# Kernel tuning notes

Hardware: AMD Instinct MI355X
Metric: run time of the kernel (lower is better)

Reference implementation:

```python
import jax, jax.numpy as jnp
import numpy as np

DIM = 320
HEADS = 8
GROUPS = 32
KV_DIM = 768


def group_norm(x, scale, bias, groups=GROUPS, eps=1e-6):
    b, c, h, w = x.shape
    xg = x.reshape(b, groups, c // groups, h, w)
    mu = xg.mean(axis=(2, 3, 4), keepdims=True)
    var = xg.var(axis=(2, 3, 4), keepdims=True)
    xg = (xg - mu) * jax.lax.rsqrt(var + eps)
    x = xg.reshape(b, c, h, w)
    return x * scale[None, :, None, None] + bias[None, :, None, None]


def layer_norm(x, scale, bias, eps=1e-5):
    mu = x.mean(-1, keepdims=True)
    var = x.var(-1, keepdims=True)
    return (x - mu) * jax.lax.rsqrt(var + eps) * scale + bias


def cross_attention(x, kv, wq, wk, wv, wo, bo, heads=HEADS):
    # weights stored as [in, out] (transposed vs torch Linear)
    b, lq, d = x.shape
    lk = kv.shape[1]
    dh = d // heads
    q = (x @ wq).reshape(b, lq, heads, dh).transpose(0, 2, 1, 3)
    k = (kv @ wk).reshape(b, lk, heads, dh).transpose(0, 2, 1, 3)
    v = (kv @ wv).reshape(b, lk, heads, dh).transpose(0, 2, 1, 3)
    scores = jnp.einsum('bhqd,bhkd->bhqk', q, k) * (dh ** -0.5)
    attn = jax.nn.softmax(scores, axis=-1)
    out = jnp.einsum('bhqk,bhkd->bhqd', attn, v)
    out = out.transpose(0, 2, 1, 3).reshape(b, lq, d)
    return out @ wo + bo


def setup_inputs() -> dict:
    key = jax.random.key(0)
    ks = jax.random.split(key, 24)
    d = DIM
    s = 0.02
    inp = {
        'q': jax.random.normal(ks[0], (2, d, 64, 64), jnp.float32),
        'kv': jax.random.normal(ks[1], (2, 77, KV_DIM), jnp.float32),
        'gn_s': jnp.ones((d,), jnp.float32),
        'gn_b': jnp.zeros((d,), jnp.float32),
        'cin_w': jax.random.normal(ks[2], (d, d), jnp.float32) * s,
        'cin_b': jnp.zeros((d,), jnp.float32),
        'ln0_s': jnp.ones((d,), jnp.float32),
        'ln0_b': jnp.zeros((d,), jnp.float32),
        'a1_wq': jax.random.normal(ks[3], (d, d), jnp.float32) * s,
        'a1_wk': jax.random.normal(ks[4], (d, d), jnp.float32) * s,
        'a1_wv': jax.random.normal(ks[5], (d, d), jnp.float32) * s,
        'a1_wo': jax.random.normal(ks[6], (d, d), jnp.float32) * s,
        'a1_bo': jnp.zeros((d,), jnp.float32),
        'ln1_s': jnp.ones((d,), jnp.float32),
        'ln1_b': jnp.zeros((d,), jnp.float32),
        'a2_wq': jax.random.normal(ks[7], (d, d), jnp.float32) * s,
        'a2_wk': jax.random.normal(ks[8], (KV_DIM, d), jnp.float32) * s,
        'a2_wv': jax.random.normal(ks[9], (KV_DIM, d), jnp.float32) * s,
        'a2_wo': jax.random.normal(ks[10], (d, d), jnp.float32) * s,
        'a2_bo': jnp.zeros((d,), jnp.float32),
        'lnA_s': jnp.ones((d,), jnp.float32),
        'lnA_b': jnp.zeros((d,), jnp.float32),
        'fc0_w': jax.random.normal(ks[11], (d, 8 * d), jnp.float32) * s,
        'fc0_b': jnp.zeros((8 * d,), jnp.float32),
        'fc1_w': jax.random.normal(ks[12], (4 * d, d), jnp.float32) * s,
        'fc1_b': jnp.zeros((d,), jnp.float32),
        'cout_w': jax.random.normal(ks[13], (d, d), jnp.float32) * s,
        'cout_b': jnp.zeros((d,), jnp.float32),
    }
    return inp


def reference(q, kv, gn_s, gn_b, cin_w, cin_b, ln0_s, ln0_b,
              a1_wq, a1_wk, a1_wv, a1_wo, a1_bo, ln1_s, ln1_b,
              a2_wq, a2_wk, a2_wv, a2_wo, a2_bo, lnA_s, lnA_b,
              fc0_w, fc0_b, fc1_w, fc1_b, cout_w, cout_b):
    b, c, h, w = q.shape
    res1 = q
    x = group_norm(q, gn_s, gn_b)
    # 1x1 conv == channel matmul
    x = jnp.einsum('bchw,co->bohw', x, cin_w) + cin_b[None, :, None, None]
    x = x.transpose(0, 2, 3, 1).reshape(b, h * w, c)
    xn = layer_norm(x, ln0_s, ln0_b)
    x = cross_attention(xn, xn, a1_wq, a1_wk, a1_wv, a1_wo, a1_bo) + x
    x = cross_attention(layer_norm(x, ln1_s, ln1_b), kv,
                        a2_wq, a2_wk, a2_wv, a2_wo, a2_bo) + x
    res2 = x
    g = layer_norm(x, lnA_s, lnA_b) @ fc0_w + fc0_b
    half = g.shape[-1] // 2
    # GEGLU: value * GELU(gate); torch nn.GELU default is exact (erf)
    g = g[..., :half] * jax.nn.gelu(g[..., half:], approximate=False)
    x = g @ fc1_w + fc1_b + res2
    x = x.reshape(b, h, w, c).transpose(0, 3, 1, 2)
    x = jnp.einsum('bchw,co->bohw', x, cout_w) + cout_b[None, :, None, None] + res1
    return x
```

## Files before the change

kernel.cpp:

```cpp
#include <hip/hip_runtime.h>
#include <math.h>

typedef short short8 __attribute__((ext_vector_type(8)));
typedef float floatx4 __attribute__((ext_vector_type(4)));
typedef unsigned short ushort_t;
typedef unsigned int uint_t;

constexpr int BATCH   = 2;
constexpr int DIM     = 320;
constexpr int NHEADS  = 8;
constexpr int DH      = 40;
constexpr int NGROUPS = 32;
constexpr int CPG     = 10;
constexpr int SPATIAL = 4096;
constexpr int ROWS    = BATCH * SPATIAL;
constexpr int KVL     = 77;
constexpr int KVD     = 768;
constexpr int FF      = 1280;
constexpr int TQ      = 128;
constexpr int SELF_PARTS = 4;

#define QK_EXP2_SCALE 0.2281259062f

__device__ __forceinline__ ushort_t f2bf(float f) {
    uint_t u = __float_as_uint(f);
    u += 0x7FFFu + ((u >> 16) & 1u);
    return (ushort_t)(u >> 16);
}
__device__ __forceinline__ float bf2f(ushort_t u) {
    return __uint_as_float(((uint_t)u) << 16);
}

__device__ __forceinline__ void gld16(const ushort_t* g, ushort_t* l) {
    __builtin_amdgcn_global_load_lds(
        (const __attribute__((address_space(1))) void*)g,
        (__attribute__((address_space(3))) void*)l, 16, 0, 0);
}

__global__ __launch_bounds__(256) void gn_partial_kernel(const float* __restrict__ q,
                                                         float* __restrict__ stats) {
    int slice = blockIdx.x, bg = blockIdx.y;
    const float* base = q + (size_t)bg * (CPG * SPATIAL) + slice * 2560;
    float s = 0.f, ss = 0.f;
#pragma unroll
    for (int j = 0; j < 10; j++) {
        float v = base[j * 256 + threadIdx.x];
        s += v; ss += v * v;
    }
    __shared__ float rs[256], rss[256];
    rs[threadIdx.x] = s; rss[threadIdx.x] = ss;
    __syncthreads();
    for (int off = 128; off > 0; off >>= 1) {
        if (threadIdx.x < off) {
            rs[threadIdx.x]  += rs[threadIdx.x + off];
            rss[threadIdx.x] += rss[threadIdx.x + off];
        }
        __syncthreads();
    }
    if (threadIdx.x == 0) {
        atomicAdd(&stats[bg * 2],     rs[0]);
        atomicAdd(&stats[bg * 2 + 1], rss[0]);
    }
}

__global__ void gn_apply_transpose_kernel(const float* __restrict__ q,
                                          const float* __restrict__ stats,
                                          const float* __restrict__ gs,
                                          const float* __restrict__ gb,
                                          ushort_t* __restrict__ out) {
    __shared__ float tile[32][33];
    int l0 = blockIdx.x * 32, c0 = blockIdx.y * 32, b = blockIdx.z;
    int tx = threadIdx.x, ty = threadIdx.y;
    int c = c0 + ty;
    int g = c / CPG;
    float s  = stats[(b * NGROUPS + g) * 2];
    float ss = stats[(b * NGROUPS + g) * 2 + 1];
    const float invn = 1.f / 40960.f;
    float mean = s * invn;
    float rstd = rsqrtf(ss * invn - mean * mean + 1e-6f);
    float v = q[((size_t)(b * DIM + c)) * SPATIAL + l0 + tx];
    tile[ty][tx] = (v - mean) * rstd * gs[c] + gb[c];
    __syncthreads();
    out[((size_t)(b * SPATIAL + l0 + ty)) * DIM + c0 + tx] = f2bf(tile[tx][ty]);
}

__global__ __launch_bounds__(256) void ln_kernel(const float* __restrict__ x,
                                                 const float* __restrict__ sc,
                                                 const float* __restrict__ bi,
                                                 ushort_t* __restrict__ out) {
    int row = blockIdx.x * 4 + (threadIdx.x >> 6);
    int lane = threadIdx.x & 63;
    const float* xr = x + (size_t)row * DIM;
    float v[5];
    float sum = 0.f, sq = 0.f;
#pragma unroll
    for (int j = 0; j < 5; j++) {
        v[j] = xr[lane + j * 64];
        sum += v[j]; sq += v[j] * v[j];
    }
#pragma unroll
    for (int off = 32; off > 0; off >>= 1) {
        sum += __shfl_down(sum, off);
        sq  += __shfl_down(sq, off);
    }
    sum = __shfl(sum, 0); sq = __shfl(sq, 0);
    float mean = sum / (float)DIM;
    float rstd = rsqrtf(sq / (float)DIM - mean * mean + 1e-5f);
#pragma unroll
    for (int j = 0; j < 5; j++) {
        int i = lane + j * 64;
        out[(size_t)row * DIM + i] = f2bf((v[j] - mean) * rstd * sc[i] + bi[i]);
    }
}

struct WSeg { const float* src; ushort_t* dst; int K; int N; int t0; };
struct WTab {
    WSeg s[12];
    const float* cvt_src; ushort_t* cvt_dst; int cvt_n; int cvt_t0;
    float* stats;
};

__global__ __launch_bounds__(256) void wtrans_all_kernel(WTab tab) {
    int bid = blockIdx.x;
    if (bid >= tab.cvt_t0) {
        int local = bid - tab.cvt_t0;
        int base = local * 8192;
#pragma unroll
        for (int j = 0; j < 32; j++) {
            int i = base + j * 256 + threadIdx.x;
            if (i < tab.cvt_n) tab.cvt_dst[i] = f2bf(tab.cvt_src[i]);
        }
        if (local == 0 && threadIdx.x < 128) tab.stats[threadIdx.x] = 0.f;
        return;
    }
    __shared__ float tile[32][33];
    int si = 0;
#pragma unroll
    for (int i = 1; i < 12; i++) if (bid >= tab.s[i].t0) si = i;
    WSeg sg = tab.s[si];
    int local = bid - sg.t0;
    int ntn = sg.N >> 5;
    int kt = local / ntn, nt = local - kt * ntn;
    int n0 = nt * 32, k0 = kt * 32;
    int tx = threadIdx.x & 31, ty8 = threadIdx.x >> 5;
    for (int r = ty8; r < 32; r += 8)
        tile[r][tx] = sg.src[(size_t)(k0 + r) * sg.N + n0 + tx];
    __syncthreads();
    for (int r = ty8; r < 32; r += 8)
        sg.dst[(size_t)(n0 + r) * sg.K + k0 + tx] = f2bf(tile[tx][r]);
}

__global__ __launch_bounds__(256) void vtrans_kernel(const ushort_t* __restrict__ src,
                                                     ushort_t* __restrict__ dst,
                                                     int stride, int headOff,
                                                     int L, int Lpad) {
    __shared__ ushort_t tile[32][41];
    int bh = blockIdx.y, b = bh >> 3, h = bh & 7;
    int l0 = blockIdx.x * 32;
    for (int idx = threadIdx.x; idx < 32 * 40; idx += 256) {
        int l = idx / 40, d = idx - l * 40;
        ushort_t v = 0;
        if (l0 + l < L)
            v = src[(size_t)(b * L + l0 + l) * stride + headOff + h * DH + d];
        tile[l][d] = v;
    }
    __syncthreads();
    for (int idx = threadIdx.x; idx < 48 * 32; idx += 256) {
        int d = idx >> 5, li = idx & 31;
        ushort_t v;
        if (d < 40)      v = tile[li][d];
        else if (d == 40) v = 0x3F80;
        else             v = 0;
        dst[((size_t)bh * 48 + d) * Lpad + l0 + li] = v;
    }
}

template <int TM>
__global__ __launch_bounds__(256) void gemm_bf16_kernel(
    const ushort_t* __restrict__ A, const ushort_t* __restrict__ Wt,
    const float* __restrict__ bias, const float* __restrict__ resid,
    float* __restrict__ Cf, ushort_t* __restrict__ Cb,
    int M, int N, int K, float qsc, int ncut)
{
    constexpr int G = TM / 64;
    __shared__ __align__(16) ushort_t As[TM][64];
    __shared__ __align__(16) ushort_t Bs[64][64];
    int tid = threadIdx.x;
    int wave = tid >> 6, lane = tid & 63;
    int l15 = tid & 15, quad = lane >> 4;
    int m0 = blockIdx.x * TM, n0 = blockIdx.y * 64;
    int lrow = lane >> 3, slot = lane & 7;
    floatx4 acc[G][4] = {};

    for (int k0 = 0; k0 < K; k0 += 64) {
#pragma unroll
        for (int t = 0; t < TM / 32; t++) {
            int task = wave * (TM / 32) + t;
            int r = task * 8 + lrow;
            int gc = slot ^ (r & 7);
            gld16(&A[(size_t)(m0 + r) * K + k0 + gc * 8], &As[task * 8][0]);
        }
#pragma unroll
        for (int t = 0; t < 2; t++) {
            int task = wave * 2 + t;
            int r = task * 8 + lrow;
            int gc = slot ^ (r & 7);
            gld16(&Wt[(size_t)(n0 + r) * K + k0 + gc * 8], &Bs[task * 8][0]);
        }
        __syncthreads();
        short8 a[G][2], b[4][2];
#pragma unroll
        for (int g = 0; g < G; g++) {
            int r = (TM / 4) * wave + 16 * g + l15;
            a[g][0] = *(const short8*)&As[r][(quad ^ (r & 7)) * 8];
            a[g][1] = *(const short8*)&As[r][((4 + quad) ^ (r & 7)) * 8];
        }
#pragma unroll
        for (int t = 0; t < 4; t++) {
            int r = 16 * t + l15;
            b[t][0] = *(const short8*)&Bs[r][(quad ^ (r & 7)) * 8];
            b[t][1] = *(const short8*)&Bs[r][((4 + quad) ^ (r & 7)) * 8];
        }
#pragma unroll
        for (int g = 0; g < G; g++)
#pragma unroll
            for (int t = 0; t < 4; t++) {
                acc[g][t] = __builtin_amdgcn_mfma_f32_16x16x32_bf16(a[g][0], b[t][0], acc[g][t], 0, 0, 0);
                acc[g][t] = __builtin_amdgcn_mfma_f32_16x16x32_bf16(a[g][1], b[t][1], acc[g][t], 0, 0, 0);
            }
        __syncthreads();
    }

#pragma unroll
    for (int g = 0; g < G; g++) {
        int mrow = m0 + (TM / 4) * wave + 16 * g + quad * 4;
#pragma unroll
        for (int t = 0; t < 4; t++) {
            int n = n0 + 16 * t + l15;
            float bv = bias ? bias[n] : 0.f;
            float sc = (n < ncut) ? qsc : 1.f;
#pragma unroll
            for (int i = 0; i < 4; i++) {
                int m = mrow + i;
                float v = acc[g][t][i] + bv;
                if (resid) v += resid[(size_t)m * N + n];
                v *= sc;
                if (Cf) Cf[(size_t)m * N + n] = v;
                if (Cb) Cb[(size_t)m * N + n] = f2bf(v);
            }
        }
    }
}

__global__ __launch_bounds__(256) void geglu128_kernel(
    const ushort_t* __restrict__ A, const ushort_t* __restrict__ Wt,
    const float* __restrict__ bias, ushort_t* __restrict__ C, int M)
{
    constexpr int K = 320;
    __shared__ __align__(16) ushort_t As[128][64];
    __shared__ __align__(16) ushort_t Bv[64][64];
    __shared__ __align__(16) ushort_t Bg[64][64];
    int tid = threadIdx.x;
    int wave = tid >> 6, lane = tid & 63;
    int l15 = tid & 15, quad = lane >> 4;
    int m0 = blockIdx.x * 128, n0 = blockIdx.y * 64;
    int lrow = lane >> 3, slot = lane & 7;
    floatx4 av[2][4] = {}, ag[2][4] = {};

    for (int k0 = 0; k0 < K; k0 += 64) {
#pragma unroll
        for (int t = 0; t < 4; t++) {
            int task = wave * 4 + t;
            int r = task * 8 + lrow;
            int gc = slot ^ (r & 7);
            gld16(&A[(size_t)(m0 + r) * K + k0 + gc * 8], &As[task * 8][0]);
        }
#pragma unroll
        for (int t = 0; t < 2; t++) {
            int task = wave * 2 + t;
            int r = task * 8 + lrow;
            int gc = slot ^ (r & 7);
            gld16(&Wt[(size_t)(n0 + r) * K + k0 + gc * 8],      &Bv[task * 8][0]);
            gld16(&Wt[(size_t)(FF + n0 + r) * K + k0 + gc * 8], &Bg[task * 8][0]);
        }
        __syncthreads();
        short8 a[2][2], bv[4][2], bg[4][2];
#pragma unroll
        for (int g = 0; g < 2; g++) {
            int r = 32 * wave + 16 * g + l15;
            a[g][0] = *(const short8*)&As[r][(quad ^ (r & 7)) * 8];
            a[g][1] = *(const short8*)&As[r][((4 + quad) ^ (r & 7)) * 8];
        }
#pragma unroll
        for (int t = 0; t < 4; t++) {
            int r = 16 * t + l15;
            bv[t][0] = *(const short8*)&Bv[r][(quad ^ (r & 7)) * 8];
            bv[t][1] = *(const short8*)&Bv[r][((4 + quad) ^ (r & 7)) * 8];
            bg[t][0] = *(const short8*)&Bg[r][(quad ^ (r & 7)) * 8];
            bg[t][1] = *(const short8*)&Bg[r][((4 + quad) ^ (r & 7)) * 8];
        }
#pragma unroll
        for (int g = 0; g < 2; g++)
#pragma unroll
            for (int t = 0; t < 4; t++) {
                av[g][t] = __builtin_amdgcn_mfma_f32_16x16x32_bf16(a[g][0], bv[t][0], av[g][t], 0, 0, 0);
                av[g][t] = __builtin_amdgcn_mfma_f32_16x16x32_bf16(a[g][1], bv[t][1], av[g][t], 0, 0, 0);
                ag[g][t] = __builtin_amdgcn_mfma_f32_16x16x32_bf16(a[g][0], bg[t][0], ag[g][t], 0, 0, 0);
                ag[g][t] = __builtin_amdgcn_mfma_f32_16x16x32_bf16(a[g][1], bg[t][1], ag[g][t], 0, 0, 0);
            }
        __syncthreads();
    }

#pragma unroll
    for (int g = 0; g < 2; g++) {
        int mrow = m0 + 32 * wave + 16 * g + quad * 4;
#pragma unroll
        for (int t = 0; t < 4; t++) {
            int n = n0 + 16 * t + l15;
            float bb = bias[n], bgte = bias[FF + n];
#pragma unroll
            for (int i = 0; i < 4; i++) {
                float val  = av[g][t][i] + bb;
                float gate = ag[g][t][i] + bgte;
                float gl = 0.5f * gate * (1.f + erff(gate * 0.70710678118654752f));
                C[(size_t)(mrow + i) * FF + n] = f2bf(val * gl);
            }
        }
    }
}

__global__ __launch_bounds__(256) void gemm_convout_kernel(
    const ushort_t* __restrict__ A, const ushort_t* __restrict__ Wt,
    const float* __restrict__ bias, const float* __restrict__ qres,
    float* __restrict__ out)
{
    constexpr int K = 320;
    __shared__ __align__(16) ushort_t As[64][64];
    __shared__ __align__(16) ushort_t Bs[64][64];
    __shared__ float Cf[64][68];
    int tid = threadIdx.x;
    int wave = tid >> 6, lane = tid & 63;
    int l15 = tid & 15, quad = lane >> 4;
    int m0 = blockIdx.x * 64, n0 = blockIdx.y * 64;
    int lrow = lane >> 3, slot = lane & 7;
    floatx4 acc[4] = {};

    for (int k0 = 0; k0 < K; k0 += 64) {
#pragma unroll
        for (int t = 0; t < 2; t++) {
            int task = wave * 2 + t;
            int r = task * 8 + lrow;
            int gc = slot ^ (r & 7);
            gld16(&A[(size_t)(m0 + r) * K + k0 + gc * 8], &As[task * 8][0]);
            gld16(&Wt[(size_t)(n0 + r) * K + k0 + gc * 8], &Bs[task * 8][0]);
        }
        __syncthreads();
        short8 a0, a1, b[4][2];
        {
            int r = 16 * wave + l15;
            a0 = *(const short8*)&As[r][(quad ^ (r & 7)) * 8];
            a1 = *(const short8*)&As[r][((4 + quad) ^ (r & 7)) * 8];
        }
#pragma unroll
        for (int t = 0; t < 4; t++) {
            int r = 16 * t + l15;
            b[t][0] = *(const short8*)&Bs[r][(quad ^ (r & 7)) * 8];
            b[t][1] = *(const short8*)&Bs[r][((4 + quad) ^ (r & 7)) * 8];
        }
#pragma unroll
        for (int t = 0; t < 4; t++) {
            acc[t] = __builtin_amdgcn_mfma_f32_16x16x32_bf16(a0, b[t][0], acc[t], 0, 0, 0);
            acc[t] = __builtin_amdgcn_mfma_f32_16x16x32_bf16(a1, b[t][1], acc[t], 0, 0, 0);
        }
        __syncthreads();
    }

#pragma unroll
    for (int t = 0; t < 4; t++) {
        int n = 16 * t + l15;
        float bv = bias[n0 + n];
        int mbase = 16 * wave + 4 * quad;
#pragma unroll
        for (int i = 0; i < 4; i++)
            Cf[n][mbase + i] = acc[t][i] + bv;
    }
    __syncthreads();
    {
        int n = tid >> 2, j = tid & 3;
        int bq = m0 >> 12;
        int l0 = m0 & 4095;
        size_t goff = ((size_t)(bq * DIM + n0 + n)) * SPATIAL + l0 + j * 16;
        const float4* qr = (const float4*)(qres + goff);
        float4* op = (float4*)(out + goff);
#pragma unroll
        for (int c = 0; c < 4; c++) {
            float4 v = *(const float4*)&Cf[n][j * 16 + c * 4];
            float4 qv = qr[c];
            v.x += qv.x; v.y += qv.y; v.z += qv.z; v.w += qv.w;
            op[c] = v;
        }
    }
}

__global__ __launch_bounds__(256) void gemm_small_kernel(
    const ushort_t* __restrict__ A, const ushort_t* __restrict__ Wt,
    ushort_t* __restrict__ Cb, int M, int N, int K)
{
    __shared__ __align__(16) ushort_t As[64][72];
    __shared__ __align__(16) ushort_t Bs[64][72];
    int tid = threadIdx.x;
    int wave = tid >> 6, l15 = tid & 15, quad = (tid & 63) >> 4;
    int m0 = blockIdx.x * 64, n0 = blockIdx.y * 64;
    floatx4 acc[4] = {};

    for (int k0 = 0; k0 < K; k0 += 64) {
#pragma unroll
        for (int p = 0; p < 2; p++) {
            int lin = p * 256 + tid;
            int r = lin >> 3, c8 = (lin & 7) * 8;
            int m = m0 + r;
            short8 avv = {};
            if (m < M) avv = *(const short8*)&A[(size_t)m * K + k0 + c8];
            *(short8*)&As[r][c8] = avv;
            *(short8*)&Bs[r][c8] = *(const short8*)&Wt[(size_t)(n0 + r) * K + k0 + c8];
        }
        __syncthreads();
        short8 a0 = *(const short8*)&As[16 * wave + l15][quad * 8];
        short8 a1 = *(const short8*)&As[16 * wave + l15][32 + quad * 8];
#pragma unroll
        for (int t = 0; t < 4; t++) {
            short8 b0 = *(const short8*)&Bs[16 * t + l15][quad * 8];
            short8 b1 = *(const short8*)&Bs[16 * t + l15][32 + quad * 8];
            acc[t] = __builtin_amdgcn_mfma_f32_16x16x32_bf16(a0, b0, acc[t], 0, 0, 0);
            acc[t] = __builtin_amdgcn_mfma_f32_16x16x32_bf16(a1, b1, acc[t], 0, 0, 0);
        }
        __syncthreads();
    }
    int mrow = m0 + 16 * wave + quad * 4;
#pragma unroll
    for (int t = 0; t < 4; t++) {
        int n = n0 + 16 * t + l15;
#pragma unroll
        for (int i = 0; i < 4; i++) {
            int m = mrow + i;
            if (m < M) Cb[(size_t)m * N + n] = f2bf(acc[t][i]);
        }
    }
}

template <int NPARTS, bool FULL>
__global__ __launch_bounds__(256) void flash_kernel(
    const ushort_t* __restrict__ Qg, const ushort_t* __restrict__ Kg,
    const ushort_t* __restrict__ VT, ushort_t* __restrict__ Og,
    ushort_t* __restrict__ Opart, float* __restrict__ Lpart,
    int sQ, int sKV, int Lpad, int nk)
{
    __shared__ __align__(16) ushort_t QPs[8][130][8];
    __shared__ __align__(16) ushort_t Ks[8][64][8];
    __shared__ __align__(16) ushort_t VsT[48][64];

    int tid = threadIdx.x;
    int wave = tid >> 6, lane = tid & 63;
    int l15 = tid & 15, quad = lane >> 4;
    int qt = blockIdx.x, h = blockIdx.y;
    int b, kp;
    if (NPARTS > 1) { b = blockIdx.z / NPARTS; kp = blockIdx.z % NPARTS; }
    else            { b = blockIdx.z;          kp = 0; }
    int q0 = qt * TQ;

    const ushort_t* Qb  = Qg + (size_t)(b * SPATIAL + q0) * sQ + h * DH;
    const ushort_t* Kb  = Kg + (size_t)b * nk * sKV + h * DH;
    const ushort_t* VTb = VT + (size_t)(b * NHEADS + h) * 48 * Lpad;

    const short8 z8 = {};
    for (int i = tid; i < 3 * 64; i += 256)
        *(short8*)&Ks[5 + (i >> 6)][i & 63][0] = z8;
    for (int i = tid; i < 3 * 130; i += 256)
        *(short8*)&QPs[5 + i / 130][i % 130][0] = z8;

    for (int t5 = wave; t5 < 10; t5 += 4) {
        int cid = t5 >> 1, half = t5 & 1;
        gld16(&Qb[(size_t)(half * 64 + lane) * sQ + cid * 8], &QPs[cid][half * 64][0]);
    }
    __syncthreads();

    short8 aq[2][2];
#pragma unroll
    for (int g = 0; g < 2; g++) {
        int r = 32 * wave + 16 * g + l15;
        aq[g][0] = *(const short8*)&QPs[quad][r][0];
        aq[g][1] = *(const short8*)&QPs[4 + quad][r][0];
    }

    ushort_t* pw = &QPs[l15 >> 3][32 * wave + 4 * quad][l15 & 7];
    const ushort_t* pr = &QPs[quad][32 * wave + l15][0];

    floatx4 o[2][3] = {};

    int ntiles_all = (nk + 63) >> 6;
    int per = ntiles_all / NPARTS;
    int t_lo = kp * per;
    int t_hi = (NPARTS > 1) ? t_lo + per : ntiles_all;

    for (int t = t_lo; t < t_hi; t++) {
        int k0 = t * 64;
        __syncthreads();
        for (int c = wave; c < 5; c += 4)
            gld16(&Kb[(size_t)(k0 + lane) * sKV + c * 8], &Ks[c][0][0]);
        for (int c = wave; c < 6; c += 4) {
            int r8 = lane >> 3;
            int gc = (lane & 7) ^ r8;
            gld16(&VTb[(size_t)(c * 8 + r8) * Lpad + k0 + gc * 8], &VsT[c * 8][0]);
        }
        __syncthreads();

        floatx4 s[2][4] = {};
#pragma unroll
        for (int tt = 0; tt < 4; tt++) {
            short8 b0 = *(const short8*)&Ks[quad][16 * tt + l15][0];
            short8 b1 = *(const short8*)&Ks[4 + quad][16 * tt + l15][0];
#pragma unroll
            for (int g = 0; g < 2; g++) {
                s[g][tt] = __builtin_amdgcn_mfma_f32_16x16x32_bf16(aq[g][0], b0, s[g][tt], 0, 0, 0);
                s[g][tt] = __builtin_amdgcn_mfma_f32_16x16x32_bf16(aq[g][1], b1, s[g][tt], 0, 0, 0);
            }
        }

#pragma unroll
        for (int g = 0; g < 2; g++) {
#pragma unroll
            for (int i = 0; i < 4; i++) {
#pragma unroll
                for (int tt = 0; tt < 4; tt++) {
                    float x = s[g][tt][i];
                    if (!FULL && (k0 + 16 * tt + l15 >= nk)) x = -1e30f;
                    float pf = __builtin_amdgcn_exp2f(x);
                    pw[tt * 2080 + g * 128 + i * 8] =
                        (ushort_t)(__float_as_uint(pf) >> 16);
                }
            }
        }

        short8 vb[3][2];
#pragma unroll
        for (int t2 = 0; t2 < 3; t2++) {
            int R = 16 * t2 + l15;
            vb[t2][0] = *(const short8*)&VsT[R][(quad ^ (l15 & 7)) * 8];
            vb[t2][1] = *(const short8*)&VsT[R][((4 + quad) ^ (l15 & 7)) * 8];
        }
#pragma unroll
        for (int g = 0; g < 2; g++) {
            short8 p0 = *(const short8*)(pr + g * 128);
            short8 p1 = *(const short8*)(pr + 4 * 1040 + g * 128);
#pragma unroll
            for (int t2 = 0; t2 < 3; t2++) {
                o[g][t2] = __builtin_amdgcn_mfma_f32_16x16x32_bf16(p0, vb[t2][0], o[g][t2], 0, 0, 0);
                o[g][t2] = __builtin_amdgcn_mfma_f32_16x16x32_bf16(p1, vb[t2][1], o[g][t2], 0, 0, 0);
            }
        }
    }

    if (NPARTS == 1) {
        float inv[2][4];
#pragma unroll
        for (int g = 0; g < 2; g++)
#pragma unroll
            for (int i = 0; i < 4; i++)
                inv[g][i] = 1.f / __shfl(o[g][2][i], (lane & 48) | 8, 64);
#pragma unroll
        for (int g = 0; g < 2; g++)
#pragma unroll
            for (int t2 = 0; t2 < 3; t2++) {
                int c = 16 * t2 + l15;
                if (c < DH) {
#pragma unroll
                    for (int i = 0; i < 4; i++) {
                        size_t row = (size_t)(b * SPATIAL + q0 + 32 * wave + 16 * g + 4 * quad + i);
                        Og[row * DIM + h * DH + c] = f2bf(o[g][t2][i] * inv[g][i]);
                    }
                }
            }
    } else {
#pragma unroll
        for (int g = 0; g < 2; g++) {
#pragma unroll
            for (int t2 = 0; t2 < 3; t2++) {
                int c = 16 * t2 + l15;
                if (c < DH) {
#pragma unroll
                    for (int i = 0; i < 4; i++) {
                        size_t row = (size_t)(b * SPATIAL + q0 + 32 * wave + 16 * g + 4 * quad + i);
                        Opart[((size_t)kp * ROWS + row) * DIM + h * DH + c] = f2bf(o[g][t2][i]);
                    }
                }
            }
            if (l15 == 8) {
#pragma unroll
                for (int i = 0; i < 4; i++) {
                    size_t row = (size_t)(b * SPATIAL + q0 + 32 * wave + 16 * g + 4 * quad + i);
                    Lpart[((size_t)kp * ROWS + row) * NHEADS + h] = o[g][2][i];
                }
            }
        }
    }
}

__global__ __launch_bounds__(320) void attn_merge_kernel(
    const ushort_t* __restrict__ Op, const float* __restrict__ Lp,
    ushort_t* __restrict__ Og)
{
    int row = blockIdx.x, c = threadIdx.x;
    int h = c / DH;
    float l = 0.f, o = 0.f;
#pragma unroll
    for (int kp = 0; kp < SELF_PARTS; kp++) {
        l += Lp[((size_t)kp * ROWS + row) * NHEADS + h];
        o += bf2f(Op[((size_t)kp * ROWS + row) * DIM + c]);
    }
    Og[(size_t)row * DIM + c] = f2bf(o / l);
}

extern "C" void kernel_launch(void* const* d_in, const int* in_sizes, int n_in,
                              void* d_out, int out_size, void* d_ws, size_t ws_size,
                              hipStream_t stream) {
    (void)in_sizes; (void)n_in; (void)out_size; (void)ws_size;
    const float* q      = (const float*)d_in[0];
    const float* kv     = (const float*)d_in[1];
    const float* gn_s   = (const float*)d_in[2];
    const float* gn_b   = (const float*)d_in[3];
    const float* cin_w  = (const float*)d_in[4];
    const float* cin_b  = (const float*)d_in[5];
    const float* ln0_s  = (const float*)d_in[6];
    const float* ln0_b  = (const float*)d_in[7];
    const float* a1_wq  = (const float*)d_in[8];
    const float* a1_wk  = (const float*)d_in[9];
    const float* a1_wv  = (const float*)d_in[10];
    const float* a1_wo  = (const float*)d_in[11];
    const float* a1_bo  = (const float*)d_in[12];
    const float* ln1_s  = (const float*)d_in[13];
    const float* ln1_b  = (const float*)d_in[14];
    const float* a2_wq  = (const float*)d_in[15];
    const float* a2_wk  = (const float*)d_in[16];
    const float* a2_wv  = (const float*)d_in[17];
    const float* a2_wo  = (const float*)d_in[18];
    const float* a2_bo  = (const float*)d_in[19];
    const float* lnA_s  = (const float*)d_in[20];
    const float* lnA_b  = (const float*)d_in[21];
    const float* fc0_w  = (const float*)d_in[22];
    const float* fc0_b  = (const float*)d_in[23];
    const float* fc1_w  = (const float*)d_in[24];
    const float* fc1_b  = (const float*)d_in[25];
    const float* cout_w = (const float*)d_in[26];
    const float* cout_b = (const float*)d_in[27];
    float* out = (float*)d_out;

    char* p = (char*)d_ws;
    auto carve = [&](size_t bytes) -> char* {
        char* r = p;
        p += (bytes + 255) & ~(size_t)255;
        return r;
    };
    float*    stats  = (float*)carve(512);
    float*    B0     = (float*)carve((size_t)ROWS * DIM * 4);
    ushort_t* gnO    = (ushort_t*)carve((size_t)ROWS * DIM * 2);
    ushort_t* ln0O   = (ushort_t*)carve((size_t)ROWS * DIM * 2);
    ushort_t* QKV    = (ushort_t*)carve((size_t)ROWS * 960 * 2);
    ushort_t* attnO  = (ushort_t*)carve((size_t)ROWS * DIM * 2);
    ushort_t* ln1O   = (ushort_t*)carve((size_t)ROWS * DIM * 2);
    ushort_t* Q2     = (ushort_t*)carve((size_t)ROWS * DIM * 2);
    ushort_t* KVc    = (ushort_t*)carve((size_t)BATCH * KVL * 640 * 2);
    ushort_t* lnAO   = (ushort_t*)carve((size_t)ROWS * DIM * 2);
    ushort_t* GLU    = (ushort_t*)carve((size_t)ROWS * FF * 2);
    ushort_t* X2     = (ushort_t*)carve((size_t)ROWS * DIM * 2);
    ushort_t* kvbf   = (ushort_t*)carve((size_t)BATCH * KVL * KVD * 2);
    ushort_t* VTs    = (ushort_t*)carve((size_t)16 * 48 * SPATIAL * 2);
    ushort_t* VTc    = (ushort_t*)carve((size_t)16 * 48 * 128 * 2);
    ushort_t* qkv_t  = (ushort_t*)carve((size_t)960 * 320 * 2);
    ushort_t* cin_t  = (ushort_t*)carve((size_t)320 * 320 * 2);
    ushort_t* a1wo_t = (ushort_t*)carve((size_t)320 * 320 * 2);
    ushort_t* a2wq_t = (ushort_t*)carve((size_t)320 * 320 * 2);
    ushort_t* kvx_t  = (ushort_t*)carve((size_t)640 * 768 * 2);
    ushort_t* a2wo_t = (ushort_t*)carve((size_t)320 * 320 * 2);
    ushort_t* fc0_t  = (ushort_t*)carve((size_t)2560 * 320 * 2);
    ushort_t* fc1_t  = (ushort_t*)carve((size_t)320 * 1280 * 2);
    ushort_t* cout_t = (ushort_t*)carve((size_t)320 * 320 * 2);
    ushort_t* Opart = GLU;
    float*    Lpart = (float*)gnO;

    auto gemm64 = [&](const ushort_t* A, const ushort_t* Wt, const float* bias,
                      const float* resid, float* Cf, ushort_t* Cb,
                      int M, int N, int K, float qsc = 1.f, int ncut = 0) {
        gemm_bf16_kernel<64><<<dim3(M / 64, N / 64), 256, 0, stream>>>(
            A, Wt, bias, resid, Cf, Cb, M, N, K, qsc, ncut);
    };
    auto gemm128 = [&](const ushort_t* A, const ushort_t* Wt, const float* bias,
                       const float* resid, float* Cf, ushort_t* Cb,
                       int M, int N, int K, float qsc = 1.f, int ncut = 0) {
        gemm_bf16_kernel<128><<<dim3(M / 128, N / 64), 256, 0, stream>>>(
            A, Wt, bias, resid, Cf, Cb, M, N, K, qsc, ncut);
    };

    {
        WTab tab;
        int t0 = 0;
        auto seg = [&](int i, const float* s, ushort_t* d, int K, int N) {
            tab.s[i] = {s, d, K, N, t0};
            t0 += (K / 32) * (N / 32);
        };
        seg(0,  cin_w,  cin_t,             320, 320);
        seg(1,  a1_wq,  qkv_t,             320, 320);
        seg(2,  a1_wk,  qkv_t + 320 * 320, 320, 320);
        seg(3,  a1_wv,  qkv_t + 640 * 320, 320, 320);
        seg(4,  a1_wo,  a1wo_t,            320, 320);
        seg(5,  a2_wq,  a2wq_t,            320, 320);
        seg(6,  a2_wk,  kvx_t,             768, 320);
        seg(7,  a2_wv,  kvx_t + 320 * 768, 768, 320);
        seg(8,  a2_wo,  a2wo_t,            320, 320);
        seg(9,  fc0_w,  fc0_t,             320, 2560);
        seg(10, fc1_w,  fc1_t,             1280, 320);
        seg(11, cout_w, cout_t,            320, 320);
        tab.cvt_src = kv; tab.cvt_dst = kvbf;
        tab.cvt_n = BATCH * KVL * KVD; tab.cvt_t0 = t0;
        tab.stats = stats;
        int ncvt_blk = (tab.cvt_n + 8191) / 8192;
        wtrans_all_kernel<<<t0 + ncvt_blk, 256, 0, stream>>>(tab);
    }

    gn_partial_kernel<<<dim3(16, 64), 256, 0, stream>>>(q, stats);
    gn_apply_transpose_kernel<<<dim3(SPATIAL / 32, DIM / 32, BATCH), dim3(32, 32), 0, stream>>>(
        q, stats, gn_s, gn_b, gnO);
    gemm64(gnO, cin_t, cin_b, nullptr, B0, nullptr, ROWS, DIM, DIM);

    ln_kernel<<<ROWS / 4, 256, 0, stream>>>(B0, ln0_s, ln0_b, ln0O);
    gemm128(ln0O, qkv_t, nullptr, nullptr, nullptr, QKV, ROWS, 960, DIM, QK_EXP2_SCALE, 320);
    vtrans_kernel<<<dim3(SPATIAL / 32, 16), 256, 0, stream>>>(QKV, VTs, 960, 640, SPATIAL, SPATIAL);
    flash_kernel<SELF_PARTS, true><<<dim3(SPATIAL / TQ, NHEADS, BATCH * SELF_PARTS), 256, 0, stream>>>(
        QKV, QKV + 320, VTs, nullptr, Opart, Lpart, 960, 960, SPATIAL, SPATIAL);
    attn_merge_kernel<<<ROWS, 320, 0, stream>>>(Opart, Lpart, attnO);
    gemm64(attnO, a1wo_t, a1_bo, B0, B0, nullptr, ROWS, DIM, DIM);

    ln_kernel<<<ROWS / 4, 256, 0, stream>>>(B0, ln1_s, ln1_b, ln1O);
    gemm64(ln1O, a2wq_t, nullptr, nullptr, nullptr, Q2, ROWS, DIM, DIM, QK_EXP2_SCALE, 320);
    gemm_small_kernel<<<dim3(3, 10), 256, 0, stream>>>(kvbf, kvx_t, KVc, BATCH * KVL, 640, KVD);
    vtrans_kernel<<<dim3(4, 16), 256, 0, stream>>>(KVc, VTc, 640, 320, KVL, 128);
    flash_kernel<1, false><<<dim3(SPATIAL / TQ, NHEADS, BATCH), 256, 0, stream>>>(
        Q2, KVc, VTc, attnO, nullptr, nullptr, 320, 640, 128, KVL);
    gemm64(attnO, a2wo_t, a2_bo, B0, B0, nullptr, ROWS, DIM, DIM);

    ln_kernel<<<ROWS / 4, 256, 0, stream>>>(B0, lnA_s, lnA_b, lnAO);
    geglu128_kernel<<<dim3(ROWS / 128, FF / 64), 256, 0, stream>>>(lnAO, fc0_t, fc0_b, GLU, ROWS);
    gemm64(GLU, fc1_t, fc1_b, B0, nullptr, X2, ROWS, DIM, FF);

    gemm_convout_kernel<<<dim3(ROWS / 64, DIM / 64), 256, 0, stream>>>(
        X2, cout_t, cout_b, q, out);
}
```

Measured before the change: 378.2 us.

## Fuse V transpose into QKV and KV projection GEMM epilogues, vectorize merge

Removes both vtrans kernels. The QKV and KV projection GEMMs now write V directly in the transposed, padded per-head layout. The constant padding rows (ones row and zeros) are filled once inside the weight-prep kernel. The attention merge kernel is vectorized to 4 elements per thread, and layernorm uses 512-thread blocks. The V-fragment loads are also hoisted earlier inside flash attention. This saves two launches and an extra read/write of V, at the cost of scattered 8-byte stores in the GEMM epilogue and added padding-init work.

```diff
diff --git a/kernel.cpp b/kernel.cpp
--- a/kernel.cpp
+++ b/kernel.cpp
@@ -4,6 +4,7 @@
 typedef short short8 __attribute__((ext_vector_type(8)));
 typedef float floatx4 __attribute__((ext_vector_type(4)));
 typedef unsigned short ushort_t;
+typedef unsigned short ushort4_t __attribute__((ext_vector_type(4)));
 typedef unsigned int uint_t;
 
 constexpr int BATCH   = 2;
@@ -84,11 +85,11 @@
     out[((size_t)(b * SPATIAL + l0 + ty)) * DIM + c0 + tx] = f2bf(tile[tx][ty]);
 }
 
-__global__ __launch_bounds__(256) void ln_kernel(const float* __restrict__ x,
+__global__ __launch_bounds__(512) void ln_kernel(const float* __restrict__ x,
                                                  const float* __restrict__ sc,
                                                  const float* __restrict__ bi,
                                                  ushort_t* __restrict__ out) {
-    int row = blockIdx.x * 4 + (threadIdx.x >> 6);
+    int row = blockIdx.x * 8 + (threadIdx.x >> 6);
     int lane = threadIdx.x & 63;
     const float* xr = x + (size_t)row * DIM;
     float v[5];
@@ -118,10 +119,33 @@
     WSeg s[12];
     const float* cvt_src; ushort_t* cvt_dst; int cvt_n; int cvt_t0;
     float* stats;
+    ushort_t* vts; int vts_t0;
+    ushort_t* vtc; int vtc_t0;
 };
 
 __global__ __launch_bounds__(256) void wtrans_all_kernel(WTab tab) {
     int bid = blockIdx.x;
+    if (bid >= tab.vtc_t0) {
+        int base = (bid - tab.vtc_t0) * 8192;
+#pragma unroll
+        for (int j = 0; j < 32; j++) {
+            int e = base + j * 256 + threadIdx.x;
+            int r = (e >> 7) % 48;
+            tab.vtc[e] = (r == 40) ? (ushort_t)0x3F80 : (ushort_t)0;
+        }
+        return;
+    }
+    if (bid >= tab.vts_t0) {
+        int base = (bid - tab.vts_t0) * 8192;
+#pragma unroll
+        for (int j = 0; j < 32; j++) {
+            int e = base + j * 256 + threadIdx.x;
+            int bh = e >> 15, r = (e >> 12) & 7, col = e & 4095;
+            tab.vts[((size_t)(bh * 48 + 40 + r) << 12) + col] =
+                (r == 0) ? (ushort_t)0x3F80 : (ushort_t)0;
+        }
+        return;
+    }
     if (bid >= tab.cvt_t0) {
         int local = bid - tab.cvt_t0;
         int base = local * 8192;
@@ -148,31 +172,6 @@
     __syncthreads();
     for (int r = ty8; r < 32; r += 8)
         sg.dst[(size_t)(n0 + r) * sg.K + k0 + tx] = f2bf(tile[tx][r]);
-}
-
-__global__ __launch_bounds__(256) void vtrans_kernel(const ushort_t* __restrict__ src,
-                                                     ushort_t* __restrict__ dst,
-                                                     int stride, int headOff,
-                                                     int L, int Lpad) {
-    __shared__ ushort_t tile[32][41];
-    int bh = blockIdx.y, b = bh >> 3, h = bh & 7;
-    int l0 = blockIdx.x * 32;
-    for (int idx = threadIdx.x; idx < 32 * 40; idx += 256) {
-        int l = idx / 40, d = idx - l * 40;
-        ushort_t v = 0;
-        if (l0 + l < L)
-            v = src[(size_t)(b * L + l0 + l) * stride + headOff + h * DH + d];
-        tile[l][d] = v;
-    }
-    __syncthreads();
-    for (int idx = threadIdx.x; idx < 48 * 32; idx += 256) {
-        int d = idx >> 5, li = idx & 31;
-        ushort_t v;
-        if (d < 40)      v = tile[li][d];
-        else if (d == 40) v = 0x3F80;
-        else             v = 0;
-        dst[((size_t)bh * 48 + d) * Lpad + l0 + li] = v;
-    }
 }
 
 template <int TM>
@@ -252,6 +251,84 @@
     }
 }
 
+__global__ __launch_bounds__(256) void gemm_qkv_kernel(
+    const ushort_t* __restrict__ A, const ushort_t* __restrict__ Wt,
+    ushort_t* __restrict__ Cqk, ushort_t* __restrict__ VTdst)
+{
+    constexpr int K = 320, N = 960;
+    __shared__ __align__(16) ushort_t As[128][64];
+    __shared__ __align__(16) ushort_t Bs[64][64];
+    int tid = threadIdx.x;
+    int wave = tid >> 6, lane = tid & 63;
+    int l15 = tid & 15, quad = lane >> 4;
+    int m0 = blockIdx.x * 128, n0 = blockIdx.y * 64;
+    int lrow = lane >> 3, slot = lane & 7;
+    floatx4 acc[2][4] = {};
+
+    for (int k0 = 0; k0 < K; k0 += 64) {
+#pragma unroll
+        for (int t = 0; t < 4; t++) {
+            int task = wave * 4 + t;
+            int r = task * 8 + lrow;
+            int gc = slot ^ (r & 7);
+            gld16(&A[(size_t)(m0 + r) * K + k0 + gc * 8], &As[task * 8][0]);
+        }
+#pragma unroll
+        for (int t = 0; t < 2; t++) {
+            int task = wave * 2 + t;
+            int r = task * 8 + lrow;
+            int gc = slot ^ (r & 7);
+            gld16(&Wt[(size_t)(n0 + r) * K + k0 + gc * 8], &Bs[task * 8][0]);
+        }
+        __syncthreads();
+        short8 a[2][2], b[4][2];
+#pragma unroll
+        for (int g = 0; g < 2; g++) {
+            int r = 32 * wave + 16 * g + l15;
+            a[g][0] = *(const short8*)&As[r][(quad ^ (r & 7)) * 8];
+            a[g][1] = *(const short8*)&As[r][((4 + quad) ^ (r & 7)) * 8];
+        }
+#pragma unroll
+        for (int t = 0; t < 4; t++) {
+            int r = 16 * t + l15;
+            b[t][0] = *(const short8*)&Bs[r][(quad ^ (r & 7)) * 8];
+            b[t][1] = *(const short8*)&Bs[r][((4 + quad) ^ (r & 7)) * 8];
+        }
+#pragma unroll
+        for (int g = 0; g < 2; g++)
+#pragma unroll
+            for (int t = 0; t < 4; t++) {
+                acc[g][t] = __builtin_amdgcn_mfma_f32_16x16x32_bf16(a[g][0], b[t][0], acc[g][t], 0, 0, 0);
+                acc[g][t] = __builtin_amdgcn_mfma_f32_16x16x32_bf16(a[g][1], b[t][1], acc[g][t], 0, 0, 0);
+            }
+        __syncthreads();
+    }
+
+    int bq = m0 >> 12;
+#pragma unroll
+    for (int g = 0; g < 2; g++) {
+        int mrow = m0 + 32 * wave + 16 * g + quad * 4;
+#pragma unroll
+        for (int t = 0; t < 4; t++) {
+            int n = n0 + 16 * t + l15;
+            if (n < 640) {
+                float sc = (n < 320) ? QK_EXP2_SCALE : 1.f;
+#pragma unroll
+                for (int i = 0; i < 4; i++)
+                    Cqk[(size_t)(mrow + i) * N + n] = f2bf(acc[g][t][i] * sc);
+            } else {
+                int hd = n - 640;
+                int h = hd / DH, d = hd - h * DH;
+                int l = (mrow & 4095);
+                ushort4_t v4;
+#pragma unroll
+                for (int i = 0; i < 4; i++) v4[i] = f2bf(acc[g][t][i]);
+                *(ushort4_t*)&VTdst[((size_t)((bq * NHEADS + h) * 48 + d) << 12) + l] = v4;
+            }
+        }
+    }
+}
+
 __global__ __launch_bounds__(256) void geglu128_kernel(
     const ushort_t* __restrict__ A, const ushort_t* __restrict__ Wt,
     const float* __restrict__ bias, ushort_t* __restrict__ C, int M)
@@ -402,9 +479,9 @@
     }
 }
 
-__global__ __launch_bounds__(256) void gemm_small_kernel(
+__global__ __launch_bounds__(256) void gemm_kvx_kernel(
     const ushort_t* __restrict__ A, const ushort_t* __restrict__ Wt,
-    ushort_t* __restrict__ Cb, int M, int N, int K)
+    ushort_t* __restrict__ Cb, ushort_t* __restrict__ VTc, int M, int N, int K)
 {
     __shared__ __align__(16) ushort_t As[64][72];
     __shared__ __align__(16) ushort_t Bs[64][72];
@@ -440,10 +517,24 @@
 #pragma unroll
     for (int t = 0; t < 4; t++) {
         int n = n0 + 16 * t + l15;
-#pragma unroll
-        for (int i = 0; i < 4; i++) {
-            int m = mrow + i;
-            if (m < M) Cb[(size_t)m * N + n] = f2bf(acc[t][i]);
+        if (n < 320) {
+#pragma unroll
+            for (int i = 0; i < 4; i++) {
+                int m = mrow + i;
+                if (m < M) Cb[(size_t)m * N + n] = f2bf(acc[t][i]);
+            }
+        } else {
+            int hd = n - 320;
+            int h = hd / DH, d = hd - h * DH;
+#pragma unroll
+            for (int i = 0; i < 4; i++) {
+                int m = mrow + i;
+                if (m < M) {
+                    int b = (m >= KVL) ? 1 : 0;
+                    int l = m - b * KVL;
+                    VTc[((size_t)((b * NHEADS + h) * 48 + d) << 7) + l] = f2bf(acc[t][i]);
+                }
+            }
         }
     }
 }
@@ -526,6 +617,14 @@
             }
         }
 
+        short8 vb[3][2];
+#pragma unroll
+        for (int t2 = 0; t2 < 3; t2++) {
+            int R = 16 * t2 + l15;
+            vb[t2][0] = *(const short8*)&VsT[R][(quad ^ (l15 & 7)) * 8];
+            vb[t2][1] = *(const short8*)&VsT[R][((4 + quad) ^ (l15 & 7)) * 8];
+        }
+
 #pragma unroll
         for (int g = 0; g < 2; g++) {
 #pragma unroll
@@ -541,13 +640,6 @@
             }
         }
 
-        short8 vb[3][2];
-#pragma unroll
-        for (int t2 = 0; t2 < 3; t2++) {
-            int R = 16 * t2 + l15;
-            vb[t2][0] = *(const short8*)&VsT[R][(quad ^ (l15 & 7)) * 8];
-            vb[t2][1] = *(const short8*)&VsT[R][((4 + quad) ^ (l15 & 7)) * 8];
-        }
 #pragma unroll
         for (int g = 0; g < 2; g++) {
             short8 p0 = *(const short8*)(pr + g * 128);
@@ -609,15 +701,24 @@
     const ushort_t* __restrict__ Op, const float* __restrict__ Lp,
     ushort_t* __restrict__ Og)
 {
-    int row = blockIdx.x, c = threadIdx.x;
+    int t = threadIdx.x;
+    int row = blockIdx.x * 4 + t / 80;
+    int c = (t % 80) * 4;
     int h = c / DH;
-    float l = 0.f, o = 0.f;
+    float l = 0.f;
+    float o[4] = {};
 #pragma unroll
     for (int kp = 0; kp < SELF_PARTS; kp++) {
         l += Lp[((size_t)kp * ROWS + row) * NHEADS + h];
-        o += bf2f(Op[((size_t)kp * ROWS + row) * DIM + c]);
-    }
-    Og[(size_t)row * DIM + c] = f2bf(o / l);
+        ushort4_t v = *(const ushort4_t*)&Op[((size_t)kp * ROWS + row) * DIM + c];
+#pragma unroll
+        for (int j = 0; j < 4; j++) o[j] += bf2f(v[j]);
+    }
+    float inv = 1.f / l;
+    ushort4_t r;
+#pragma unroll
+    for (int j = 0; j < 4; j++) r[j] = f2bf(o[j] * inv);
+    *(ushort4_t*)&Og[(size_t)row * DIM + c] = r;
 }
 
 extern "C" void kernel_launch(void* const* d_in, const int* in_sizes, int n_in,
@@ -693,12 +794,6 @@
         gemm_bf16_kernel<64><<<dim3(M / 64, N / 64), 256, 0, stream>>>(
             A, Wt, bias, resid, Cf, Cb, M, N, K, qsc, ncut);
     };
-    auto gemm128 = [&](const ushort_t* A, const ushort_t* Wt, const float* bias,
-                       const float* resid, float* Cf, ushort_t* Cb,
-                       int M, int N, int K, float qsc = 1.f, int ncut = 0) {
-        gemm_bf16_kernel<128><<<dim3(M / 128, N / 64), 256, 0, stream>>>(
-            A, Wt, bias, resid, Cf, Cb, M, N, K, qsc, ncut);
-    };
 
     {
         WTab tab;
@@ -722,8 +817,11 @@
         tab.cvt_src = kv; tab.cvt_dst = kvbf;
         tab.cvt_n = BATCH * KVL * KVD; tab.cvt_t0 = t0;
         tab.stats = stats;
-        int ncvt_blk = (tab.cvt_n + 8191) / 8192;
-        wtrans_all_kernel<<<t0 + ncvt_blk, 256, 0, stream>>>(tab);
+        int ncvt = (tab.cvt_n + 8191) / 8192;
+        tab.vts = VTs; tab.vts_t0 = t0 + ncvt;
+        tab.vtc = VTc; tab.vtc_t0 = tab.vts_t0 + 64;
+        int nblk = tab.vtc_t0 + 12;
+        wtrans_all_kernel<<<nblk, 256, 0, stream>>>(tab);
     }
 
     gn_partial_kernel<<<dim3(16, 64), 256, 0, stream>>>(q, stats);
@@ -731,23 +829,21 @@
         q, stats, gn_s, gn_b, gnO);
     gemm64(gnO, cin_t, cin_b, nullptr, B0, nullptr, ROWS, DIM, DIM);
 
-    ln_kernel<<<ROWS / 4, 256, 0, stream>>>(B0, ln0_s, ln0_b, ln0O);
-    gemm128(ln0O, qkv_t, nullptr, nullptr, nullptr, QKV, ROWS, 960, DIM, QK_EXP2_SCALE, 320);
-    vtrans_kernel<<<dim3(SPATIAL / 32, 16), 256, 0, stream>>>(QKV, VTs, 960, 640, SPATIAL, SPATIAL);
+    ln_kernel<<<ROWS / 8, 512, 0, stream>>>(B0, ln0_s, ln0_b, ln0O);
+    gemm_qkv_kernel<<<dim3(ROWS / 128, 960 / 64), 256, 0, stream>>>(ln0O, qkv_t, QKV, VTs);
     flash_kernel<SELF_PARTS, true><<<dim3(SPATIAL / TQ, NHEADS, BATCH * SELF_PARTS), 256, 0, stream>>>(
         QKV, QKV + 320, VTs, nullptr, Opart, Lpart, 960, 960, SPATIAL, SPATIAL);
-    attn_merge_kernel<<<ROWS, 320, 0, stream>>>(Opart, Lpart, attnO);
+    attn_merge_kernel<<<ROWS / 4, 320, 0, stream>>>(Opart, Lpart, attnO);
     gemm64(attnO, a1wo_t, a1_bo, B0, B0, nullptr, ROWS, DIM, DIM);
 
-    ln_kernel<<<ROWS / 4, 256, 0, stream>>>(B0, ln1_s, ln1_b, ln1O);
+    ln_kernel<<<ROWS / 8, 512, 0, stream>>>(B0, ln1_s, ln1_b, ln1O);
     gemm64(ln1O, a2wq_t, nullptr, nullptr, nullptr, Q2, ROWS, DIM, DIM, QK_EXP2_SCALE, 320);
-    gemm_small_kernel<<<dim3(3, 10), 256, 0, stream>>>(kvbf, kvx_t, KVc, BATCH * KVL, 640, KVD);
-    vtrans_kernel<<<dim3(4, 16), 256, 0, stream>>>(KVc, VTc, 640, 320, KVL, 128);
+    gemm_kvx_kernel<<<dim3(3, 10), 256, 0, stream>>>(kvbf, kvx_t, KVc, VTc, BATCH * KVL, 640, KVD);
     flash_kernel<1, false><<<dim3(SPATIAL / TQ, NHEADS, BATCH), 256, 0, stream>>>(
         Q2, KVc, VTc, attnO, nullptr, nullptr, 320, 640, 128, KVL);
     gemm64(attnO, a2wo_t, a2_bo, B0, B0, nullptr, ROWS, DIM, DIM);
 
-    ln_kernel<<<ROWS / 4, 256, 0, stream>>>(B0, lnA_s, lnA_b, lnAO);
+    ln_kernel<<<ROWS / 8, 512, 0, stream>>>(B0, lnA_s, lnA_b, lnAO);
     geglu128_kernel<<<dim3(ROWS / 128, FF / 64), 256, 0, stream>>>(lnAO, fc0_t, fc0_b, GLU, ROWS);
     gemm64(GLU, fc1_t, fc1_b, B0, nullptr, X2, ROWS, DIM, FF);
 
```

After: 358.3 us. -5.3%, faster.
